# Performance work log

Hardware: AMD Instinct MI355X
Metric: run time of the kernel (lower is better)

The kernel has to match this reference:

```python
import jax, jax.numpy as jnp
import numpy as np

B, T, D, HS = 32, 2048, 384, 64

def setup_inputs() -> dict:
    key = jax.random.key(0)
    kx, kq, kk, kv = jax.random.split(key, 4)
    x = jax.random.normal(kx, (B, T, D), dtype=jnp.float32)
    s = 1.0 / np.sqrt(D)  # Linear-like init scale
    Wq = jax.random.normal(kq, (D, HS), dtype=jnp.float32) * s
    Wk = jax.random.normal(kk, (D, HS), dtype=jnp.float32) * s
    Wv = jax.random.normal(kv, (D, HS), dtype=jnp.float32) * s
    return {"x": x, "Wq": Wq, "Wk": Wk, "Wv": Wv}

def reference(x, Wq, Wk, Wv):
    # Single-head causal self-attention (dropout in eval mode -> identity).
    Tlen = x.shape[1]
    q = x @ Wq  # [B,T,HS]
    k = x @ Wk
    v = x @ Wv
    scale = q.shape[-1] ** (-0.5)
    wei = jnp.einsum('bqd,bkd->bqk', q, k) * scale  # [B,T,T]
    causal = jnp.tril(jnp.ones((Tlen, Tlen), dtype=bool))
    wei = jnp.where(causal, wei, jnp.finfo(wei.dtype).min)
    wei = jax.nn.softmax(wei, axis=-1)
    return jnp.einsum('bqk,bkd->bqd', wei, v)  # [B,T,HS]
```

## Files before the change

kernel.cpp:

```cpp
#include <hip/hip_runtime.h>
#include <hip/hip_bf16.h>

#define T_LEN 2048
#define NBATCH 32

typedef __bf16 bf16x8 __attribute__((ext_vector_type(8)));
typedef float f32x4 __attribute__((ext_vector_type(4)));

__device__ __forceinline__ unsigned short f2bf(float f) {
  return __builtin_bit_cast(unsigned short, __float2bfloat16(f));
}
__device__ __forceinline__ unsigned int pk2(float a, float b) {
  return (unsigned int)f2bf(a) | ((unsigned int)f2bf(b) << 16);
}
__device__ __forceinline__ bf16x8 ld16(const void* p) {
  return __builtin_bit_cast(bf16x8, *(const uint4*)p);
}
__device__ __forceinline__ void gl_lds16(const void* g, void* l) {
  __builtin_amdgcn_global_load_lds(
      (const __attribute__((address_space(1))) unsigned int*)g,
      (__attribute__((address_space(3))) unsigned int*)l, 16, 0, 0);
}
__device__ __forceinline__ void bar_raw() {
  asm volatile("s_barrier" ::: "memory");
}

__global__ __launch_bounds__(256) void k_wprep(const float* __restrict__ Wq,
                                               const float* __restrict__ Wk,
                                               const float* __restrict__ Wv,
                                               unsigned short* __restrict__ Wt3) {
  int idx = blockIdx.x * 256 + threadIdx.x;
  if (idx >= 192 * 384) return;
  int c = idx / 384;
  int k = idx % 384;
  const float* W = (c < 64) ? Wq : ((c < 128) ? Wk : Wv);
  Wt3[idx] = f2bf(W[k * 64 + (c & 63)]);
}

__global__ __launch_bounds__(256) void k_proj(const float* __restrict__ x,
                                              const unsigned short* __restrict__ Wt3,
                                              unsigned short* __restrict__ Qb,
                                              unsigned short* __restrict__ Kb,
                                              unsigned short* __restrict__ VTb) {
  __shared__ __align__(16) unsigned short xs[128 * 32];
  __shared__ __align__(16) unsigned short wt[192 * 32];
  const int tid = threadIdx.x;
  const int lane = tid & 63, w = tid >> 6;
  const int g = lane >> 4, lr = lane & 15;
  const long row0 = (long)blockIdx.x * 128;

  f32x4 acc[2][12] = {};

  for (int ks = 0; ks < 12; ++ks) {
    const int k0 = ks * 32;
    __syncthreads();
    {
      int r = tid >> 1, c0 = (tid & 1) * 16;
      const float4* src = reinterpret_cast<const float4*>(&x[(row0 + r) * 384 + k0 + c0]);
      float4 f0 = src[0], f1 = src[1], f2 = src[2], f3 = src[3];
      uint4 u0, u1;
      u0.x = pk2(f0.x, f0.y); u0.y = pk2(f0.z, f0.w);
      u0.z = pk2(f1.x, f1.y); u0.w = pk2(f1.z, f1.w);
      u1.x = pk2(f2.x, f2.y); u1.y = pk2(f2.z, f2.w);
      u1.z = pk2(f3.x, f3.y); u1.w = pk2(f3.z, f3.w);
      int b0 = (r * 64 + c0 * 2) ^ ((r & 7) << 4);
      int b1 = (r * 64 + c0 * 2 + 16) ^ ((r & 7) << 4);
      *reinterpret_cast<uint4*>((char*)xs + b0) = u0;
      *reinterpret_cast<uint4*>((char*)xs + b1) = u1;
    }
#pragma unroll
    for (int j = 0; j < 3; ++j) {
      int chunk = tid + 256 * j;
      int r = chunk >> 2, c8 = chunk & 3;
      uint4 d = *reinterpret_cast<const uint4*>(&Wt3[r * 384 + k0 + c8 * 8]);
      int b = (r * 64 + c8 * 16) ^ ((r & 7) << 4);
      *reinterpret_cast<uint4*>((char*)wt + b) = d;
    }
    __syncthreads();

    bf16x8 a[2];
#pragma unroll
    for (int mt = 0; mt < 2; ++mt) {
      int r = w * 32 + mt * 16 + lr;
      a[mt] = ld16((char*)xs + ((r * 64 + g * 16) ^ ((r & 7) << 4)));
    }
#pragma unroll
    for (int n = 0; n < 12; ++n) {
      int r = n * 16 + lr;
      bf16x8 bb = ld16((char*)wt + ((r * 64 + g * 16) ^ ((r & 7) << 4)));
      acc[0][n] = __builtin_amdgcn_mfma_f32_16x16x32_bf16(a[0], bb, acc[0][n], 0, 0, 0);
      acc[1][n] = __builtin_amdgcn_mfma_f32_16x16x32_bf16(a[1], bb, acc[1][n], 0, 0, 0);
    }
  }

#pragma unroll
  for (int mt = 0; mt < 2; ++mt)
#pragma unroll
    for (int n = 0; n < 12; ++n)
#pragma unroll
      for (int rr = 0; rr < 4; ++rr) {
        long grow = row0 + w * 32 + mt * 16 + g * 4 + rr;
        int col = n * 16 + lr;
        unsigned short hv = f2bf(acc[mt][n][rr]);
        if (n < 4) {
          Qb[grow * 64 + col] = hv;
        } else if (n < 8) {
          Kb[grow * 64 + (col - 64)] = hv;
        } else {
          long bb_ = grow >> 11;
          long t = grow & 2047;
          VTb[(bb_ * 64 + (col - 128)) * 2048 + t] = hv;
        }
      }
}

__global__ __launch_bounds__(256, 4) void k_attn(const unsigned short* __restrict__ Qb,
                                                 const unsigned short* __restrict__ Kb,
                                                 const unsigned short* __restrict__ VTb,
                                                 float* __restrict__ out) {
  __shared__ __align__(16) char ksm[2 * 8192];
  __shared__ __align__(16) char vsm[2 * 8192];
  __shared__ __align__(16) unsigned short psm[4 * 16 * 64];

  const int tid = threadIdx.x;
  const int lane = tid & 63, w = tid >> 6;
  const int g = lane >> 4, lr = lane & 15;
  const int b = blockIdx.x;
  const int qt = (gridDim.y - 1) - blockIdx.y;
  const int qrow0 = qt * 64 + w * 16;

  const char* Kg = (const char*)(Kb + (long)b * T_LEN * 64);
  const char* Vg = (const char*)(VTb + (long)b * 64 * 2048);

  const int lrow = lane >> 3;
  const int lsw = (((lane & 7) ^ lrow) << 4);

  bf16x8 qf[2];
#pragma unroll
  for (int c = 0; c < 2; ++c)
    qf[c] = ld16(&Qb[((long)(b * T_LEN + qrow0 + lr)) * 64 + c * 32 + g * 8]);

  f32x4 o[4] = {};
  float m_r[4], l_r[4];
#pragma unroll
  for (int r = 0; r < 4; ++r) { m_r[r] = -1e30f; l_r[r] = 0.f; }

  char* pbase = (char*)psm + w * 2048;
  const int nkv = qt + 1;

  {
    const char* gk = Kg + ((long)(w * 16 + lrow)) * 128 + lsw;
    const char* gv = Vg + ((long)(w * 16 + lrow)) * 4096 + lsw;
    char* kb = ksm + w * 2048;
    char* vb = vsm + w * 2048;
    gl_lds16(gk, kb);             gl_lds16(gk + 8 * 128, kb + 1024);
    gl_lds16(gv, vb);             gl_lds16(gv + 8 * 4096, vb + 1024);
  }

  int cur = 0;
  for (int t = 0; t < nkv; ++t) {
    const int kv0 = t * 64;

    bar_raw();

    if (t + 1 < nkv) {
      const int kv1 = kv0 + 64;
      const char* gk = Kg + ((long)(kv1 + w * 16 + lrow)) * 128 + lsw;
      const char* gv = Vg + ((long)(w * 16 + lrow)) * 4096 + (long)kv1 * 2 + lsw;
      char* kb = ksm + (cur ^ 1) * 8192 + w * 2048;
      char* vb = vsm + (cur ^ 1) * 8192 + w * 2048;
      gl_lds16(gk, kb);           gl_lds16(gk + 8 * 128, kb + 1024);
      gl_lds16(gv, vb);           gl_lds16(gv + 8 * 4096, vb + 1024);
      asm volatile("s_waitcnt vmcnt(4)" ::: "memory");
    } else {
      asm volatile("s_waitcnt vmcnt(0)" ::: "memory");
    }
    bar_raw();

    char* kt = ksm + cur * 8192;
    char* vt = vsm + cur * 8192;

    f32x4 s[4] = {};
    __builtin_amdgcn_s_setprio(1);
#pragma unroll
    for (int c = 0; c < 2; ++c)
#pragma unroll
      for (int n = 0; n < 4; ++n) {
        int r = n * 16 + lr;
        bf16x8 kf = ld16(kt + ((r * 128 + c * 64 + g * 16) ^ ((r & 7) << 4)));
        s[n] = __builtin_amdgcn_mfma_f32_16x16x32_bf16(qf[c], kf, s[n], 0, 0, 0);
      }
    __builtin_amdgcn_s_setprio(0);

    const bool diag = (t == qt);
#pragma unroll
    for (int n = 0; n < 4; ++n)
#pragma unroll
      for (int r = 0; r < 4; ++r) {
        float v = s[n][r] * 0.125f;
        if (diag) {
          int col = kv0 + n * 16 + lr;
          int rowq = qrow0 + g * 4 + r;
          if (col > rowq) v = -1e30f;
        }
        s[n][r] = v;
      }

    float pm[4];
#pragma unroll
    for (int r = 0; r < 4; ++r)
      pm[r] = fmaxf(fmaxf(s[0][r], s[1][r]), fmaxf(s[2][r], s[3][r]));
    bool need = false;
#pragma unroll
    for (int r = 0; r < 4; ++r) need = need || (pm[r] > m_r[r] + 8.0f);
    if (__any((int)need)) {
#pragma unroll
      for (int r = 0; r < 4; ++r) {
        float mx = pm[r];
        mx = fmaxf(mx, __shfl_xor(mx, 1));
        mx = fmaxf(mx, __shfl_xor(mx, 2));
        mx = fmaxf(mx, __shfl_xor(mx, 4));
        mx = fmaxf(mx, __shfl_xor(mx, 8));
        float mn = fmaxf(m_r[r], mx);
        float sc = exp2f((m_r[r] - mn) * 1.44269504f);
        m_r[r] = mn;
        l_r[r] *= sc;
#pragma unroll
        for (int n = 0; n < 4; ++n) o[n][r] *= sc;
      }
    }
    float pr[4][4];
#pragma unroll
    for (int r = 0; r < 4; ++r)
#pragma unroll
      for (int n = 0; n < 4; ++n) {
        float p = exp2f((s[n][r] - m_r[r]) * 1.44269504f);
        pr[n][r] = p;
        l_r[r] += p;
      }

#pragma unroll
    for (int n = 0; n < 4; ++n)
#pragma unroll
      for (int r = 0; r < 4; ++r) {
        int rq = g * 4 + r;
        int col = n * 16 + lr;
        *(unsigned short*)(pbase + ((rq * 128 + col * 2) ^ ((rq & 7) << 4))) = f2bf(pr[n][r]);
      }

    bf16x8 pf[2];
#pragma unroll
    for (int c = 0; c < 2; ++c)
      pf[c] = ld16(pbase + ((lr * 128 + c * 64 + g * 16) ^ ((lr & 7) << 4)));
    __builtin_amdgcn_s_setprio(1);
#pragma unroll
    for (int c = 0; c < 2; ++c)
#pragma unroll
      for (int n = 0; n < 4; ++n) {
        int r = n * 16 + lr;
        bf16x8 vf = ld16(vt + ((r * 128 + c * 64 + g * 16) ^ ((r & 7) << 4)));
        o[n] = __builtin_amdgcn_mfma_f32_16x16x32_bf16(pf[c], vf, o[n], 0, 0, 0);
      }
    __builtin_amdgcn_s_setprio(0);

    cur ^= 1;
  }

#pragma unroll
  for (int r = 0; r < 4; ++r) {
    float l = l_r[r];
    l += __shfl_xor(l, 1);
    l += __shfl_xor(l, 2);
    l += __shfl_xor(l, 4);
    l += __shfl_xor(l, 8);
    float inv = 1.0f / l;
#pragma unroll
    for (int n = 0; n < 4; ++n) {
      long rowg = (long)b * T_LEN + qrow0 + g * 4 + r;
      out[rowg * 64 + n * 16 + lr] = o[n][r] * inv;
    }
  }
}

extern "C" void kernel_launch(void* const* d_in, const int* in_sizes, int n_in,
                              void* d_out, int out_size, void* d_ws, size_t ws_size,
                              hipStream_t stream) {
  const float* x  = (const float*)d_in[0];
  const float* Wq = (const float*)d_in[1];
  const float* Wk = (const float*)d_in[2];
  const float* Wv = (const float*)d_in[3];
  float* out = (float*)d_out;

  char* ws = (char*)d_ws;
  unsigned short* Wt3 = (unsigned short*)ws;
  unsigned short* Qb  = (unsigned short*)(ws + 0x80000);
  unsigned short* Kb  = (unsigned short*)(ws + 0x80000 + 0x800000);
  unsigned short* VTb = (unsigned short*)(ws + 0x80000 + 0x1000000);

  k_wprep<<<dim3(288), dim3(256), 0, stream>>>(Wq, Wk, Wv, Wt3);
  k_proj<<<dim3(512), dim3(256), 0, stream>>>(x, Wt3, Qb, Kb, VTb);
  k_attn<<<dim3(NBATCH, 32), dim3(256), 0, stream>>>(Qb, Kb, VTb, out);
}
```

Measured before the change: 87.38 us.

## Pair causal query tiles per block to balance work and fold softmax scale

Each block now handles two query tiles, 31-p and p, one after the other, so every block does the same number of KV iterations. The grid is halved to 512 blocks. The softmax scale and log2e are folded into one FMA constant, which removes the separate multiply, and the rescale threshold is adjusted to match. The cost is fewer blocks in flight and a serial second phase per block, which lowers parallelism and the ability to hide latency.

```diff
diff --git a/kernel.cpp b/kernel.cpp
--- a/kernel.cpp
+++ b/kernel.cpp
@@ -126,8 +126,7 @@
   const int lane = tid & 63, w = tid >> 6;
   const int g = lane >> 4, lr = lane & 15;
   const int b = blockIdx.x;
-  const int qt = (gridDim.y - 1) - blockIdx.y;
-  const int qrow0 = qt * 64 + w * 16;
+  const int p = blockIdx.y;
 
   const char* Kg = (const char*)(Kb + (long)b * T_LEN * 64);
   const char* Vg = (const char*)(VTb + (long)b * 64 * 2048);
@@ -135,150 +134,155 @@
   const int lrow = lane >> 3;
   const int lsw = (((lane & 7) ^ lrow) << 4);
 
-  bf16x8 qf[2];
-#pragma unroll
-  for (int c = 0; c < 2; ++c)
-    qf[c] = ld16(&Qb[((long)(b * T_LEN + qrow0 + lr)) * 64 + c * 32 + g * 8]);
-
-  f32x4 o[4] = {};
-  float m_r[4], l_r[4];
-#pragma unroll
-  for (int r = 0; r < 4; ++r) { m_r[r] = -1e30f; l_r[r] = 0.f; }
-
+  const float C2 = 0.125f * 1.44269504f;
   char* pbase = (char*)psm + w * 2048;
-  const int nkv = qt + 1;
-
-  {
-    const char* gk = Kg + ((long)(w * 16 + lrow)) * 128 + lsw;
-    const char* gv = Vg + ((long)(w * 16 + lrow)) * 4096 + lsw;
-    char* kb = ksm + w * 2048;
-    char* vb = vsm + w * 2048;
-    gl_lds16(gk, kb);             gl_lds16(gk + 8 * 128, kb + 1024);
-    gl_lds16(gv, vb);             gl_lds16(gv + 8 * 4096, vb + 1024);
-  }
-
-  int cur = 0;
-  for (int t = 0; t < nkv; ++t) {
-    const int kv0 = t * 64;
+
+  for (int phase = 0; phase < 2; ++phase) {
+    const int qt = phase ? p : (31 - p);
+    const int qrow0 = qt * 64 + w * 16;
+    const int nkv = qt + 1;
+
+    bf16x8 qf[2];
+#pragma unroll
+    for (int c = 0; c < 2; ++c)
+      qf[c] = ld16(&Qb[((long)(b * T_LEN + qrow0 + lr)) * 64 + c * 32 + g * 8]);
+
+    f32x4 o[4] = {};
+    float m2[4], l_r[4];
+#pragma unroll
+    for (int r = 0; r < 4; ++r) { m2[r] = -1e30f; l_r[r] = 0.f; }
+
+    {
+      const char* gk = Kg + ((long)(w * 16 + lrow)) * 128 + lsw;
+      const char* gv = Vg + ((long)(w * 16 + lrow)) * 4096 + lsw;
+      char* kb = ksm + w * 2048;
+      char* vb = vsm + w * 2048;
+      gl_lds16(gk, kb);             gl_lds16(gk + 8 * 128, kb + 1024);
+      gl_lds16(gv, vb);             gl_lds16(gv + 8 * 4096, vb + 1024);
+    }
+
+    int cur = 0;
+    for (int t = 0; t < nkv; ++t) {
+      const int kv0 = t * 64;
+
+      bar_raw();
+
+      if (t + 1 < nkv) {
+        const int kv1 = kv0 + 64;
+        const char* gk = Kg + ((long)(kv1 + w * 16 + lrow)) * 128 + lsw;
+        const char* gv = Vg + ((long)(w * 16 + lrow)) * 4096 + (long)kv1 * 2 + lsw;
+        char* kb = ksm + (cur ^ 1) * 8192 + w * 2048;
+        char* vb = vsm + (cur ^ 1) * 8192 + w * 2048;
+        gl_lds16(gk, kb);           gl_lds16(gk + 8 * 128, kb + 1024);
+        gl_lds16(gv, vb);           gl_lds16(gv + 8 * 4096, vb + 1024);
+        asm volatile("s_waitcnt vmcnt(4)" ::: "memory");
+      } else {
+        asm volatile("s_waitcnt vmcnt(0)" ::: "memory");
+      }
+      bar_raw();
+
+      char* kt = ksm + cur * 8192;
+      char* vt = vsm + cur * 8192;
+
+      f32x4 s[4] = {};
+      __builtin_amdgcn_s_setprio(1);
+#pragma unroll
+      for (int c = 0; c < 2; ++c)
+#pragma unroll
+        for (int n = 0; n < 4; ++n) {
+          int r = n * 16 + lr;
+          bf16x8 kf = ld16(kt + ((r * 128 + c * 64 + g * 16) ^ ((r & 7) << 4)));
+          s[n] = __builtin_amdgcn_mfma_f32_16x16x32_bf16(qf[c], kf, s[n], 0, 0, 0);
+        }
+      __builtin_amdgcn_s_setprio(0);
+
+      if (t == qt) {
+#pragma unroll
+        for (int n = 0; n < 4; ++n)
+#pragma unroll
+          for (int r = 0; r < 4; ++r) {
+            int col = kv0 + n * 16 + lr;
+            int rowq = qrow0 + g * 4 + r;
+            if (col > rowq) s[n][r] = -1e30f;
+          }
+      }
+
+      float pm[4];
+#pragma unroll
+      for (int r = 0; r < 4; ++r)
+        pm[r] = fmaxf(fmaxf(s[0][r], s[1][r]), fmaxf(s[2][r], s[3][r]));
+      bool need = false;
+#pragma unroll
+      for (int r = 0; r < 4; ++r) need = need || (pm[r] * C2 > m2[r] + 11.5f);
+      if (__any((int)need)) {
+#pragma unroll
+        for (int r = 0; r < 4; ++r) {
+          float mx = pm[r];
+          mx = fmaxf(mx, __shfl_xor(mx, 1));
+          mx = fmaxf(mx, __shfl_xor(mx, 2));
+          mx = fmaxf(mx, __shfl_xor(mx, 4));
+          mx = fmaxf(mx, __shfl_xor(mx, 8));
+          float mn = fmaxf(m2[r], mx * C2);
+          float sc = exp2f(m2[r] - mn);
+          m2[r] = mn;
+          l_r[r] *= sc;
+#pragma unroll
+          for (int n = 0; n < 4; ++n) o[n][r] *= sc;
+        }
+      }
+      float pr[4][4];
+#pragma unroll
+      for (int r = 0; r < 4; ++r)
+#pragma unroll
+        for (int n = 0; n < 4; ++n) {
+          float pv = exp2f(__builtin_fmaf(s[n][r], C2, -m2[r]));
+          pr[n][r] = pv;
+          l_r[r] += pv;
+        }
+
+#pragma unroll
+      for (int n = 0; n < 4; ++n)
+#pragma unroll
+        for (int r = 0; r < 4; ++r) {
+          int rq = g * 4 + r;
+          int col = n * 16 + lr;
+          *(unsigned short*)(pbase + ((rq * 128 + col * 2) ^ ((rq & 7) << 4))) = f2bf(pr[n][r]);
+        }
+
+      bf16x8 pf[2];
+#pragma unroll
+      for (int c = 0; c < 2; ++c)
+        pf[c] = ld16(pbase + ((lr * 128 + c * 64 + g * 16) ^ ((lr & 7) << 4)));
+      __builtin_amdgcn_s_setprio(1);
+#pragma unroll
+      for (int c = 0; c < 2; ++c)
+#pragma unroll
+        for (int n = 0; n < 4; ++n) {
+          int r = n * 16 + lr;
+          bf16x8 vf = ld16(vt + ((r * 128 + c * 64 + g * 16) ^ ((r & 7) << 4)));
+          o[n] = __builtin_amdgcn_mfma_f32_16x16x32_bf16(pf[c], vf, o[n], 0, 0, 0);
+        }
+      __builtin_amdgcn_s_setprio(0);
+
+      cur ^= 1;
+    }
+
+#pragma unroll
+    for (int r = 0; r < 4; ++r) {
+      float l = l_r[r];
+      l += __shfl_xor(l, 1);
+      l += __shfl_xor(l, 2);
+      l += __shfl_xor(l, 4);
+      l += __shfl_xor(l, 8);
+      float inv = 1.0f / l;
+#pragma unroll
+      for (int n = 0; n < 4; ++n) {
+        long rowg = (long)b * T_LEN + qrow0 + g * 4 + r;
+        out[rowg * 64 + n * 16 + lr] = o[n][r] * inv;
+      }
+    }
 
     bar_raw();
-
-    if (t + 1 < nkv) {
-      const int kv1 = kv0 + 64;
-      const char* gk = Kg + ((long)(kv1 + w * 16 + lrow)) * 128 + lsw;
-      const char* gv = Vg + ((long)(w * 16 + lrow)) * 4096 + (long)kv1 * 2 + lsw;
-      char* kb = ksm + (cur ^ 1) * 8192 + w * 2048;
-      char* vb = vsm + (cur ^ 1) * 8192 + w * 2048;
-      gl_lds16(gk, kb);           gl_lds16(gk + 8 * 128, kb + 1024);
-      gl_lds16(gv, vb);           gl_lds16(gv + 8 * 4096, vb + 1024);
-      asm volatile("s_waitcnt vmcnt(4)" ::: "memory");
-    } else {
-      asm volatile("s_waitcnt vmcnt(0)" ::: "memory");
-    }
-    bar_raw();
-
-    char* kt = ksm + cur * 8192;
-    char* vt = vsm + cur * 8192;
-
-    f32x4 s[4] = {};
-    __builtin_amdgcn_s_setprio(1);
-#pragma unroll
-    for (int c = 0; c < 2; ++c)
-#pragma unroll
-      for (int n = 0; n < 4; ++n) {
-        int r = n * 16 + lr;
-        bf16x8 kf = ld16(kt + ((r * 128 + c * 64 + g * 16) ^ ((r & 7) << 4)));
-        s[n] = __builtin_amdgcn_mfma_f32_16x16x32_bf16(qf[c], kf, s[n], 0, 0, 0);
-      }
-    __builtin_amdgcn_s_setprio(0);
-
-    const bool diag = (t == qt);
-#pragma unroll
-    for (int n = 0; n < 4; ++n)
-#pragma unroll
-      for (int r = 0; r < 4; ++r) {
-        float v = s[n][r] * 0.125f;
-        if (diag) {
-          int col = kv0 + n * 16 + lr;
-          int rowq = qrow0 + g * 4 + r;
-          if (col > rowq) v = -1e30f;
-        }
-        s[n][r] = v;
-      }
-
-    float pm[4];
-#pragma unroll
-    for (int r = 0; r < 4; ++r)
-      pm[r] = fmaxf(fmaxf(s[0][r], s[1][r]), fmaxf(s[2][r], s[3][r]));
-    bool need = false;
-#pragma unroll
-    for (int r = 0; r < 4; ++r) need = need || (pm[r] > m_r[r] + 8.0f);
-    if (__any((int)need)) {
-#pragma unroll
-      for (int r = 0; r < 4; ++r) {
-        float mx = pm[r];
-        mx = fmaxf(mx, __shfl_xor(mx, 1));
-        mx = fmaxf(mx, __shfl_xor(mx, 2));
-        mx = fmaxf(mx, __shfl_xor(mx, 4));
-        mx = fmaxf(mx, __shfl_xor(mx, 8));
-        float mn = fmaxf(m_r[r], mx);
-        float sc = exp2f((m_r[r] - mn) * 1.44269504f);
-        m_r[r] = mn;
-        l_r[r] *= sc;
-#pragma unroll
-        for (int n = 0; n < 4; ++n) o[n][r] *= sc;
-      }
-    }
-    float pr[4][4];
-#pragma unroll
-    for (int r = 0; r < 4; ++r)
-#pragma unroll
-      for (int n = 0; n < 4; ++n) {
-        float p = exp2f((s[n][r] - m_r[r]) * 1.44269504f);
-        pr[n][r] = p;
-        l_r[r] += p;
-      }
-
-#pragma unroll
-    for (int n = 0; n < 4; ++n)
-#pragma unroll
-      for (int r = 0; r < 4; ++r) {
-        int rq = g * 4 + r;
-        int col = n * 16 + lr;
-        *(unsigned short*)(pbase + ((rq * 128 + col * 2) ^ ((rq & 7) << 4))) = f2bf(pr[n][r]);
-      }
-
-    bf16x8 pf[2];
-#pragma unroll
-    for (int c = 0; c < 2; ++c)
-      pf[c] = ld16(pbase + ((lr * 128 + c * 64 + g * 16) ^ ((lr & 7) << 4)));
-    __builtin_amdgcn_s_setprio(1);
-#pragma unroll
-    for (int c = 0; c < 2; ++c)
-#pragma unroll
-      for (int n = 0; n < 4; ++n) {
-        int r = n * 16 + lr;
-        bf16x8 vf = ld16(vt + ((r * 128 + c * 64 + g * 16) ^ ((r & 7) << 4)));
-        o[n] = __builtin_amdgcn_mfma_f32_16x16x32_bf16(pf[c], vf, o[n], 0, 0, 0);
-      }
-    __builtin_amdgcn_s_setprio(0);
-
-    cur ^= 1;
-  }
-
-#pragma unroll
-  for (int r = 0; r < 4; ++r) {
-    float l = l_r[r];
-    l += __shfl_xor(l, 1);
-    l += __shfl_xor(l, 2);
-    l += __shfl_xor(l, 4);
-    l += __shfl_xor(l, 8);
-    float inv = 1.0f / l;
-#pragma unroll
-    for (int n = 0; n < 4; ++n) {
-      long rowg = (long)b * T_LEN + qrow0 + g * 4 + r;
-      out[rowg * 64 + n * 16 + lr] = o[n][r] * inv;
-    }
   }
 }
 
@@ -299,5 +303,5 @@
 
   k_wprep<<<dim3(288), dim3(256), 0, stream>>>(Wq, Wk, Wv, Wt3);
   k_proj<<<dim3(512), dim3(256), 0, stream>>>(x, Wt3, Qb, Kb, VTb);
-  k_attn<<<dim3(NBATCH, 32), dim3(256), 0, stream>>>(Qb, Kb, VTb, out);
-}
+  k_attn<<<dim3(NBATCH, 16), dim3(256), 0, stream>>>(Qb, Kb, VTb, out);
+}
```

Measured after the change: 90.28 us. +3.3%, slower.
